# Performance work log

Measured on AMD Instinct MI355X. Metric: run time of the kernel, lower is better.

## Reference

```python
import jax, jax.numpy as jnp
import numpy as np

D_MODEL = 1024
NHEAD = 16
HEAD_DIM = D_MODEL // NHEAD
D_FF = 4096
EPS = 1e-5


def _linear(x, w, b):
    # torch Linear: y = x @ W^T + b, W is [out, in]
    return x @ w.T + b


def _layernorm(x, g, b):
    mu = jnp.mean(x, axis=-1, keepdims=True)
    var = jnp.var(x, axis=-1, keepdims=True)
    return (x - mu) * jax.lax.rsqrt(var + EPS) * g + b


def setup_inputs() -> dict:
    key = jax.random.key(0)
    ks = jax.random.split(key, 16)
    s = 0.02
    inp = {
        'x': jax.random.normal(ks[0], (2048, D_MODEL), jnp.float32),
        'q_in_w': s * jax.random.normal(ks[1], (D_MODEL, D_MODEL), jnp.float32),
        'q_in_b': jnp.zeros((D_MODEL,), jnp.float32),
        'k_in_w': s * jax.random.normal(ks[2], (D_MODEL, D_MODEL), jnp.float32),
        'k_in_b': jnp.zeros((D_MODEL,), jnp.float32),
        'v_in_w': s * jax.random.normal(ks[3], (D_MODEL, D_MODEL), jnp.float32),
        'v_in_b': jnp.zeros((D_MODEL,), jnp.float32),
        'out_w': s * jax.random.normal(ks[4], (D_MODEL, D_MODEL), jnp.float32),
        'out_b': jnp.zeros((D_MODEL,), jnp.float32),
        'ffn1_w': s * jax.random.normal(ks[5], (D_FF, D_MODEL), jnp.float32),
        'ffn1_b': jnp.zeros((D_FF,), jnp.float32),
        'ffn2_w': s * jax.random.normal(ks[6], (D_MODEL, D_FF), jnp.float32),
        'ffn2_b': jnp.zeros((D_MODEL,), jnp.float32),
        'n1_g': jnp.ones((D_MODEL,), jnp.float32),
        'n1_b': jnp.zeros((D_MODEL,), jnp.float32),
        'n2_g': jnp.ones((D_MODEL,), jnp.float32),
        'n2_b': jnp.zeros((D_MODEL,), jnp.float32),
        'q_out_w': s * jax.random.normal(ks[7], (D_MODEL, D_MODEL), jnp.float32),
        'q_out_b': jnp.zeros((D_MODEL,), jnp.float32),
        'k_out_w': s * jax.random.normal(ks[8], (D_MODEL, D_MODEL), jnp.float32),
        'k_out_b': jnp.zeros((D_MODEL,), jnp.float32),
        'v_out_w': s * jax.random.normal(ks[9], (D_MODEL, D_MODEL), jnp.float32),
        'v_out_b': jnp.zeros((D_MODEL,), jnp.float32),
        'seq_length': 2048,
    }
    return inp


def reference(x, q_in_w, q_in_b, k_in_w, k_in_b, v_in_w, v_in_b,
              out_w, out_b, ffn1_w, ffn1_b, ffn2_w, ffn2_b,
              n1_g, n1_b, n2_g, n2_b,
              q_out_w, q_out_b, k_out_w, k_out_b, v_out_w, v_out_b,
              seq_length):
    S = seq_length
    # --- is_first: batched in-projections (replaces per-token loop + cat) ---
    q_buf = _linear(x, q_in_w, q_in_b)   # [S, D]
    k_buf = _linear(x, k_in_w, k_in_b)
    v_buf = _linear(x, v_in_w, v_in_b)
    prev_layer_input = x

    # --- multi-head attention (non-causal, no mask) ---
    q = q_buf.reshape(S, NHEAD, HEAD_DIM).transpose(1, 0, 2)  # [H, S, Dh]
    k = k_buf.reshape(S, NHEAD, HEAD_DIM).transpose(1, 0, 2)
    v = v_buf.reshape(S, NHEAD, HEAD_DIM).transpose(1, 0, 2)
    scale = 1.0 / np.sqrt(HEAD_DIM).astype(np.float32)
    scores = jnp.einsum('hqd,hkd->hqk', q, k) * scale        # [H, S, S]
    attn = jax.nn.softmax(scores, axis=-1)
    ctx = jnp.einsum('hqk,hkd->hqd', attn, v)                # [H, S, Dh]
    attn_output = ctx.transpose(1, 0, 2).reshape(S, D_MODEL)  # [S, D]

    # --- post-norm residual blocks (batched over tokens) ---
    h = _linear(attn_output, out_w, out_b)
    h = _layernorm(prev_layer_input + h, n1_g, n1_b)
    ff = _linear(jax.nn.relu(_linear(h, ffn1_w, ffn1_b)), ffn2_w, ffn2_b)
    y = _layernorm(h + ff, n2_g, n2_b)                        # [S, D]

    # --- not is_last: out-projections for the next layer ---
    q_next = _linear(y, q_out_w, q_out_b)
    k_next = _linear(y, k_out_w, k_out_b)
    v_next = _linear(y, v_out_w, v_out_b)
    return (q_next, k_next, v_next, y)
```

## Files before the change

### kernel.cpp

```cpp
#include <hip/hip_runtime.h>
#include <math.h>

#define SEQ   2048
#define DM    1024
#define NH    16
#define DH    64
#define DFF   4096
#define KVSPLIT 4

typedef __bf16 bf16;
using bf16x8 = __attribute__((ext_vector_type(8))) __bf16;
using f32x4  = __attribute__((ext_vector_type(4))) float;

__device__ __forceinline__ unsigned short f2bfu(float f) {
    unsigned int u = __float_as_uint(f);
    u += 0x7FFF + ((u >> 16) & 1);
    return (unsigned short)(u >> 16);
}
__device__ __forceinline__ bf16 f2bf(float f) {
    unsigned short s = f2bfu(f);
    return __builtin_bit_cast(bf16, s);
}

__device__ __forceinline__ void gll16(const bf16* g, bf16* lds_base) {
    __builtin_amdgcn_global_load_lds(
        (const __attribute__((address_space(1))) unsigned int*)g,
        (__attribute__((address_space(3))) unsigned int*)lds_base, 16, 0, 0);
}

__global__ __launch_bounds__(256) void conv_k(const float* __restrict__ src,
                                              bf16* __restrict__ dst, int n) {
    int i = (blockIdx.x * 256 + threadIdx.x) * 4;
    if (i >= n) return;
    float4 v = *(const float4*)(src + i);
    ushort4 o;
    o.x = f2bfu(v.x); o.y = f2bfu(v.y); o.z = f2bfu(v.z); o.w = f2bfu(v.w);
    *(ushort4*)((unsigned short*)dst + i) = o;
}

struct ConvSeg  { const float* src; bf16* dst; int n; };
struct ConvSegs { ConvSeg s[6]; };

__global__ __launch_bounds__(256) void conv_multi_k(ConvSegs cs) {
    ConvSeg sg = cs.s[blockIdx.y];
    int i = (blockIdx.x * 256 + threadIdx.x) * 4;
    if (i >= sg.n) return;
    float4 v = *(const float4*)(sg.src + i);
    ushort4 o;
    o.x = f2bfu(v.x); o.y = f2bfu(v.y); o.z = f2bfu(v.z); o.w = f2bfu(v.w);
    *(ushort4*)((unsigned short*)sg.dst + i) = o;
}

struct GemmPtrs {
    const bf16* W[3];
    const float* bias[3];
    float* out32[3];
    bf16*  out16[3];
};

template<int BM, int BN>
__global__ __launch_bounds__(256) void gemm_bf16_k(
    const bf16* __restrict__ A, GemmPtrs p, int N, int K, int relu)
{
    constexpr int TM = BM / 32;
    constexpr int TN = BN / 32;
    __shared__ bf16 As[BM][32];
    __shared__ bf16 Ws[BN][32];

    const int t    = threadIdx.x;
    const int lane = t & 63;
    const int wave = t >> 6;
    const int quad = lane >> 4;
    const int l15  = lane & 15;
    const int wm   = (wave >> 1) * (BM / 2);
    const int wn   = (wave & 1) * (BN / 2);
    const int m0   = blockIdx.y * BM;
    const int n0   = blockIdx.x * BN;
    const bf16* __restrict__ W = p.W[blockIdx.z];

    f32x4 acc[TM][TN];
    #pragma unroll
    for (int i = 0; i < TM; ++i)
        #pragma unroll
        for (int j = 0; j < TN; ++j)
            acc[i][j] = f32x4{0.f, 0.f, 0.f, 0.f};

    for (int k0 = 0; k0 < K; k0 += 32) {
        #pragma unroll
        for (int s = 0; s < BM / 64; ++s) {
            int base = s * 256 + wave * 64;
            int idx  = base + lane;
            gll16(A + (long)(m0 + (idx >> 2)) * K + k0 + (idx & 3) * 8,
                  &As[0][0] + (long)base * 8);
        }
        #pragma unroll
        for (int s = 0; s < BN / 64; ++s) {
            int base = s * 256 + wave * 64;
            int idx  = base + lane;
            gll16(W + (long)(n0 + (idx >> 2)) * K + k0 + (idx & 3) * 8,
                  &Ws[0][0] + (long)base * 8);
        }
        __syncthreads();

        bf16x8 a[TM], b[TN];
        #pragma unroll
        for (int i = 0; i < TM; ++i)
            a[i] = *(const bf16x8*)&As[wm + i * 16 + l15][quad * 8];
        #pragma unroll
        for (int j = 0; j < TN; ++j)
            b[j] = *(const bf16x8*)&Ws[wn + j * 16 + l15][quad * 8];
        #pragma unroll
        for (int i = 0; i < TM; ++i)
            #pragma unroll
            for (int j = 0; j < TN; ++j)
                acc[i][j] = __builtin_amdgcn_mfma_f32_16x16x32_bf16(
                    a[i], b[j], acc[i][j], 0, 0, 0);
        __syncthreads();
    }

    float* o32 = p.out32[blockIdx.z];
    bf16*  o16 = p.out16[blockIdx.z];
    const float* bias = p.bias[blockIdx.z];
    #pragma unroll
    for (int j = 0; j < TN; ++j) {
        int n = n0 + wn + j * 16 + l15;
        float bv = bias[n];
        #pragma unroll
        for (int i = 0; i < TM; ++i) {
            #pragma unroll
            for (int r = 0; r < 4; ++r) {
                int m = m0 + wm + i * 16 + quad * 4 + r;
                float v = acc[i][j][r] + bv;
                if (relu) v = fmaxf(v, 0.f);
                if (o32) o32[(long)m * N + n] = v;
                if (o16) o16[(long)m * N + n] = f2bf(v);
            }
        }
    }
}

template<int BM, int BN, int KS>
__global__ __launch_bounds__(256) void gemm_splitk_k(
    const bf16* __restrict__ A, const bf16* __restrict__ W,
    float* __restrict__ part, int N, int K)
{
    constexpr int TM = BM / 32;
    constexpr int TN = BN / 32;
    __shared__ bf16 As[BM][32];
    __shared__ bf16 Ws[BN][32];

    const int t    = threadIdx.x;
    const int lane = t & 63;
    const int wave = t >> 6;
    const int quad = lane >> 4;
    const int l15  = lane & 15;
    const int wm   = (wave >> 1) * (BM / 2);
    const int wn   = (wave & 1) * (BN / 2);
    const int m0   = blockIdx.y * BM;
    const int n0   = blockIdx.x * BN;
    const int Kp   = K / KS;
    const int klo  = blockIdx.z * Kp;
    const long MN  = (long)gridDim.y * BM * N;

    f32x4 acc[TM][TN];
    #pragma unroll
    for (int i = 0; i < TM; ++i)
        #pragma unroll
        for (int j = 0; j < TN; ++j)
            acc[i][j] = f32x4{0.f, 0.f, 0.f, 0.f};

    for (int k0 = klo; k0 < klo + Kp; k0 += 32) {
        #pragma unroll
        for (int s = 0; s < BM / 64; ++s) {
            int base = s * 256 + wave * 64;
            int idx  = base + lane;
            gll16(A + (long)(m0 + (idx >> 2)) * K + k0 + (idx & 3) * 8,
                  &As[0][0] + (long)base * 8);
        }
        #pragma unroll
        for (int s = 0; s < BN / 64; ++s) {
            int base = s * 256 + wave * 64;
            int idx  = base + lane;
            gll16(W + (long)(n0 + (idx >> 2)) * K + k0 + (idx & 3) * 8,
                  &Ws[0][0] + (long)base * 8);
        }
        __syncthreads();

        bf16x8 a[TM], b[TN];
        #pragma unroll
        for (int i = 0; i < TM; ++i)
            a[i] = *(const bf16x8*)&As[wm + i * 16 + l15][quad * 8];
        #pragma unroll
        for (int j = 0; j < TN; ++j)
            b[j] = *(const bf16x8*)&Ws[wn + j * 16 + l15][quad * 8];
        #pragma unroll
        for (int i = 0; i < TM; ++i)
            #pragma unroll
            for (int j = 0; j < TN; ++j)
                acc[i][j] = __builtin_amdgcn_mfma_f32_16x16x32_bf16(
                    a[i], b[j], acc[i][j], 0, 0, 0);
        __syncthreads();
    }

    float* o = part + (long)blockIdx.z * MN;
    #pragma unroll
    for (int j = 0; j < TN; ++j) {
        int n = n0 + wn + j * 16 + l15;
        #pragma unroll
        for (int i = 0; i < TM; ++i)
            #pragma unroll
            for (int r = 0; r < 4; ++r) {
                int m = m0 + wm + i * 16 + quad * 4 + r;
                o[(long)m * N + n] = acc[i][j][r];
            }
    }
}

__global__ __launch_bounds__(256) void attn_mfma_k(
    const bf16* __restrict__ Q, const bf16* __restrict__ Kg,
    const bf16* __restrict__ Vg, bf16* __restrict__ Opart,
    float* __restrict__ lpart)
{
    __shared__ bf16 Kb[64][72];
    __shared__ bf16 Vt[64][72];
    __shared__ bf16 Pw[4][16][76];

    const int t    = threadIdx.x;
    const int lane = t & 63;
    const int wave = t >> 6;
    const int quad = lane >> 4;
    const int l15  = lane & 15;
    const int h    = blockIdx.y;
    const int q0   = blockIdx.x * 64;
    const int spl  = blockIdx.z;
    const int cb   = h * DH;
    const long SD  = (long)SEQ * DM;

    const int qrow = q0 + wave * 16 + l15;
    bf16x8 aQ[2];
    #pragma unroll
    for (int kh = 0; kh < 2; ++kh)
        aQ[kh] = *(const bf16x8*)(Q + (long)qrow * DM + cb + kh * 32 + quad * 8);

    bf16 oneb = f2bf(l15 == 0 ? 1.0f : 0.0f);
    bf16x8 bOnes;
    #pragma unroll
    for (int j = 0; j < 8; ++j) bOnes[j] = oneb;

    f32x4 o_acc[4], l_acc;
    #pragma unroll
    for (int dt = 0; dt < 4; ++dt) o_acc[dt] = f32x4{0.f, 0.f, 0.f, 0.f};
    l_acc = f32x4{0.f, 0.f, 0.f, 0.f};

    const float SCL = 0.18033688f;
    const int kv_lo = spl * (SEQ / KVSPLIT);
    const int kv_hi = kv_lo + SEQ / KVSPLIT;

    for (int kv0 = kv_lo; kv0 < kv_hi; kv0 += 64) {
        __syncthreads();
        #pragma unroll
        for (int s = 0; s < 2; ++s) {
            int idx = t + s * 256;
            int key = idx >> 3;
            int dg  = idx & 7;
            *(uint4*)&Kb[key][dg * 8] =
                *(const uint4*)(Kg + (long)(kv0 + key) * DM + cb + dg * 8);
            bf16x8 vv = *(const bf16x8*)(Vg + (long)(kv0 + key) * DM + cb + dg * 8);
            int swz = key ^ (dg * 8);
            #pragma unroll
            for (int j = 0; j < 8; ++j) Vt[dg * 8 + j][swz] = vv[j];
        }
        __syncthreads();

        f32x4 s4[4];
        #pragma unroll
        for (int kt = 0; kt < 4; ++kt) {
            bf16x8 b0 = *(const bf16x8*)&Kb[kt * 16 + l15][quad * 8];
            bf16x8 b1 = *(const bf16x8*)&Kb[kt * 16 + l15][32 + quad * 8];
            f32x4 s = f32x4{0.f, 0.f, 0.f, 0.f};
            s = __builtin_amdgcn_mfma_f32_16x16x32_bf16(aQ[0], b0, s, 0, 0, 0);
            s = __builtin_amdgcn_mfma_f32_16x16x32_bf16(aQ[1], b1, s, 0, 0, 0);
            s4[kt] = s;
        }

        #pragma unroll
        for (int kt = 0; kt < 4; ++kt) {
            #pragma unroll
            for (int r = 0; r < 4; ++r) {
                float pv = exp2f(s4[kt][r] * SCL);
                unsigned u = __float_as_uint(pv) + 0x8000u;
                Pw[wave][quad * 4 + r][kt * 16 + l15] =
                    __builtin_bit_cast(bf16, (unsigned short)(u >> 16));
            }
        }
        bf16x8 aP[2];
        aP[0] = *(const bf16x8*)&Pw[wave][l15][quad * 8];
        aP[1] = *(const bf16x8*)&Pw[wave][l15][32 + quad * 8];

        l_acc = __builtin_amdgcn_mfma_f32_16x16x32_bf16(aP[0], bOnes, l_acc, 0, 0, 0);
        l_acc = __builtin_amdgcn_mfma_f32_16x16x32_bf16(aP[1], bOnes, l_acc, 0, 0, 0);

        #pragma unroll
        for (int dt = 0; dt < 4; ++dt) {
            int d   = dt * 16 + l15;
            int dgr = d >> 3;
            bf16x8 v0 = *(const bf16x8*)&Vt[d][((quad) ^ dgr) * 8];
            bf16x8 v1 = *(const bf16x8*)&Vt[d][((4 + quad) ^ dgr) * 8];
            o_acc[dt] = __builtin_amdgcn_mfma_f32_16x16x32_bf16(aP[0], v0, o_acc[dt], 0, 0, 0);
            o_acc[dt] = __builtin_amdgcn_mfma_f32_16x16x32_bf16(aP[1], v1, o_acc[dt], 0, 0, 0);
        }
    }

    #pragma unroll
    for (int r = 0; r < 4; ++r) {
        int row = q0 + wave * 16 + quad * 4 + r;
        #pragma unroll
        for (int dt = 0; dt < 4; ++dt)
            Opart[(long)spl * SD + (long)row * DM + cb + dt * 16 + l15] =
                f2bf(o_acc[dt][r]);
        if (l15 == 0)
            lpart[((long)spl * NH + h) * SEQ + row] = l_acc[r];
    }
}

__global__ __launch_bounds__(256) void attn_reduce_k(
    const bf16* __restrict__ Opart, const float* __restrict__ lpart,
    bf16* __restrict__ O)
{
    const long SD = (long)SEQ * DM;
    long i = ((long)blockIdx.x * 256 + threadIdx.x) * 8;
    int row = (int)(i / DM);
    int h   = (int)((i % DM) / DH);

    float l = 0.f;
    #pragma unroll
    for (int k = 0; k < KVSPLIT; ++k)
        l += lpart[((long)k * NH + h) * SEQ + row];
    float inv = 1.f / l;

    float acc[8] = {};
    #pragma unroll
    for (int k = 0; k < KVSPLIT; ++k) {
        bf16x8 v = *(const bf16x8*)(Opart + (long)k * SD + i);
        #pragma unroll
        for (int j = 0; j < 8; ++j) acc[j] += (float)v[j];
    }
    bf16x8 o;
    #pragma unroll
    for (int j = 0; j < 8; ++j) o[j] = f2bf(acc[j] * inv);
    *(bf16x8*)(O + i) = o;
}

template<int NS>
__global__ __launch_bounds__(256) void ln_red_k(
    const float* __restrict__ part, const float* __restrict__ bias,
    const float* __restrict__ res, const float* __restrict__ g,
    const float* __restrict__ b, float* __restrict__ out32,
    bf16* __restrict__ out16)
{
    const long SD = (long)SEQ * DM;
    const int row = blockIdx.x;
    const int t   = threadIdx.x;
    const long off = (long)row * DM + (t << 2);

    float4 v = *(const float4*)(res + off);
    float4 bv0 = *(const float4*)(bias + (t << 2));
    v.x += bv0.x; v.y += bv0.y; v.z += bv0.z; v.w += bv0.w;
    #pragma unroll
    for (int z = 0; z < NS; ++z) {
        float4 pz = *(const float4*)(part + z * SD + off);
        v.x += pz.x; v.y += pz.y; v.z += pz.z; v.w += pz.w;
    }

    float s1 = v.x + v.y + v.z + v.w;
    float s2 = v.x * v.x + v.y * v.y + v.z * v.z + v.w * v.w;
    #pragma unroll
    for (int off2 = 32; off2 > 0; off2 >>= 1) {
        s1 += __shfl_xor(s1, off2);
        s2 += __shfl_xor(s2, off2);
    }
    __shared__ float red[8];
    int wid = t >> 6, lid = t & 63;
    if (lid == 0) { red[wid] = s1; red[4 + wid] = s2; }
    __syncthreads();
    s1 = red[0] + red[1] + red[2] + red[3];
    s2 = red[4] + red[5] + red[6] + red[7];

    float mu   = s1 * (1.f / DM);
    float var  = s2 * (1.f / DM) - mu * mu;
    float rstd = rsqrtf(var + 1e-5f);

    float4 gv = *(const float4*)(g + (t << 2));
    float4 bv = *(const float4*)(b + (t << 2));
    float4 ov;
    ov.x = (v.x - mu) * rstd * gv.x + bv.x;
    ov.y = (v.y - mu) * rstd * gv.y + bv.y;
    ov.z = (v.z - mu) * rstd * gv.z + bv.z;
    ov.w = (v.w - mu) * rstd * gv.w + bv.w;
    if (out32) *(float4*)(out32 + off) = ov;
    if (out16) {
        ushort4 o;
        o.x = f2bfu(ov.x); o.y = f2bfu(ov.y); o.z = f2bfu(ov.z); o.w = f2bfu(ov.w);
        *(ushort4*)((unsigned short*)out16 + off) = o;
    }
}

extern "C" void kernel_launch(void* const* d_in, const int* in_sizes, int n_in,
                              void* d_out, int out_size, void* d_ws, size_t ws_size,
                              hipStream_t stream)
{
    const float* x       = (const float*)d_in[0];
    const float* q_in_w  = (const float*)d_in[1];
    const float* q_in_b  = (const float*)d_in[2];
    const float* k_in_w  = (const float*)d_in[3];
    const float* k_in_b  = (const float*)d_in[4];
    const float* v_in_w  = (const float*)d_in[5];
    const float* v_in_b  = (const float*)d_in[6];
    const float* out_w   = (const float*)d_in[7];
    const float* out_b   = (const float*)d_in[8];
    const float* ffn1_w  = (const float*)d_in[9];
    const float* ffn1_b  = (const float*)d_in[10];
    const float* ffn2_w  = (const float*)d_in[11];
    const float* ffn2_b  = (const float*)d_in[12];
    const float* n1_g    = (const float*)d_in[13];
    const float* n1_b    = (const float*)d_in[14];
    const float* n2_g    = (const float*)d_in[15];
    const float* n2_b    = (const float*)d_in[16];
    const float* q_out_w = (const float*)d_in[17];
    const float* q_out_b = (const float*)d_in[18];
    const float* k_out_w = (const float*)d_in[19];
    const float* k_out_b = (const float*)d_in[20];
    const float* v_out_w = (const float*)d_in[21];
    const float* v_out_b = (const float*)d_in[22];

    float* out = (float*)d_out;
    const long SD = (long)SEQ * DM;
    const long MB = 1024 * 1024;

    char* w = (char*)d_ws;
    bf16*  xbf   = (bf16*)(w);
    float* lpart = (float*)(w);
    bf16*  qb    = (bf16*)(w + 4  * MB);
    bf16*  kb    = (bf16*)(w + 8  * MB);
    bf16*  vb    = (bf16*)(w + 12 * MB);
    bf16*  atnb  = (bf16*)(w + 16 * MB);
    float* h32   = (float*)(w);
    bf16*  h16   = (bf16*)(w + 8  * MB);
    float* P2    = (float*)(w + 8  * MB);
    bf16*  Opart = (bf16*)(w + 20 * MB);
    float* P1    = (float*)(w + 20 * MB);
    bf16*  f1    = (bf16*)(w + 24 * MB);
    bf16*  wqi   = (bf16*)(w + 32 * MB);
    bf16*  wki   = (bf16*)(w + 34 * MB);
    bf16*  wvi   = (bf16*)(w + 36 * MB);
    bf16*  wo    = (bf16*)(w + 38 * MB);
    bf16*  wf1   = (bf16*)(w + 40 * MB);
    bf16*  wf2   = (bf16*)(w + 40 * MB);
    bf16*  wqo   = (bf16*)(w + 24 * MB);
    bf16*  wko   = (bf16*)(w + 26 * MB);
    bf16*  wvo   = (bf16*)(w + 28 * MB);
    bf16*  ybf   = (bf16*)(w + 30 * MB);
    float* y32   = out + 3 * SD;

    dim3 blk(256);
    const int DD = DM * DM;

    {
        ConvSegs cs;
        cs.s[0] = {x,      xbf, (int)SD};
        cs.s[1] = {q_in_w, wqi, DD};
        cs.s[2] = {k_in_w, wki, DD};
        cs.s[3] = {v_in_w, wvi, DD};
        cs.s[4] = {out_w,  wo,  DD};
        cs.s[5] = {ffn1_w, wf1, DM * DFF};
        conv_multi_k<<<dim3(DM * DFF / 1024, 6), blk, 0, stream>>>(cs);
    }

    {
        GemmPtrs p{};
        p.W[0] = wqi; p.W[1] = wki; p.W[2] = wvi;
        p.bias[0] = q_in_b; p.bias[1] = k_in_b; p.bias[2] = v_in_b;
        p.out16[0] = qb; p.out16[1] = kb; p.out16[2] = vb;
        gemm_bf16_k<128, 64><<<dim3(DM / 64, SEQ / 128, 3), blk, 0, stream>>>(
            xbf, p, DM, DM, 0);
    }

    attn_mfma_k<<<dim3(SEQ / 64, NH, KVSPLIT), blk, 0, stream>>>(
        qb, kb, vb, Opart, lpart);
    attn_reduce_k<<<dim3((int)(SD / 2048)), blk, 0, stream>>>(Opart, lpart, atnb);

    gemm_splitk_k<64, 128, 2><<<dim3(DM / 128, SEQ / 64, 2), blk, 0, stream>>>(
        atnb, wo, P1, DM, DM);

    ln_red_k<2><<<SEQ, blk, 0, stream>>>(P1, out_b, x, n1_g, n1_b, h32, h16);

    {
        GemmPtrs p{};
        p.W[0] = wf1; p.bias[0] = ffn1_b; p.out16[0] = f1;
        gemm_bf16_k<128, 64><<<dim3(DFF / 64, SEQ / 128, 1), blk, 0, stream>>>(
            h16, p, DFF, DM, 1);
    }

    conv_k<<<dim3(DM * DFF / 1024), blk, 0, stream>>>(ffn2_w, wf2, DM * DFF);

    gemm_splitk_k<64, 128, 2><<<dim3(DM / 128, SEQ / 64, 2), blk, 0, stream>>>(
        f1, wf2, P2, DM, DFF);

    {
        ConvSegs cs;
        cs.s[0] = {q_out_w, wqo, DD};
        cs.s[1] = {k_out_w, wko, DD};
        cs.s[2] = {v_out_w, wvo, DD};
        cs.s[3] = cs.s[0]; cs.s[4] = cs.s[0]; cs.s[5] = cs.s[0];
        conv_multi_k<<<dim3(DD / 1024, 3), blk, 0, stream>>>(cs);
    }

    ln_red_k<2><<<SEQ, blk, 0, stream>>>(P2, ffn2_b, h32, n2_g, n2_b, y32, ybf);

    {
        GemmPtrs p{};
        p.W[0] = wqo; p.W[1] = wko; p.W[2] = wvo;
        p.bias[0] = q_out_b; p.bias[1] = k_out_b; p.bias[2] = v_out_b;
        p.out32[0] = out; p.out32[1] = out + SD; p.out32[2] = out + 2 * SD;
        gemm_bf16_k<128, 64><<<dim3(DM / 64, SEQ / 128, 3), blk, 0, stream>>>(
            ybf, p, DM, DM, 0);
    }
}
```

Measured before the change: 356.9 us.

## Compute transposed scores in registers to drop K and P shared-memory staging

The attention kernel now computes S^T by putting K as the MFMA A operand, loaded straight from global memory, and Q as the B operand. The score fragments are then already in the register layout the P·V MFMA needs, so the P round-trip through shared memory and the K shared-memory tile go away. The V shared-memory layout is permuted on write to match the new key ordering. The row sum comes from register adds plus cross-lane shuffles instead of an extra MFMA against a ones vector. In exchange, K is re-read from global or cache by every wave and the P operand is converted per element in registers.

```diff
diff --git a/kernel.cpp b/kernel.cpp
--- a/kernel.cpp
+++ b/kernel.cpp
@@ -221,9 +221,7 @@
     const bf16* __restrict__ Vg, bf16* __restrict__ Opart,
     float* __restrict__ lpart)
 {
-    __shared__ bf16 Kb[64][72];
     __shared__ bf16 Vt[64][72];
-    __shared__ bf16 Pw[4][16][76];
 
     const int t    = threadIdx.x;
     const int lane = t & 63;
@@ -237,20 +235,15 @@
     const long SD  = (long)SEQ * DM;
 
     const int qrow = q0 + wave * 16 + l15;
-    bf16x8 aQ[2];
+    bf16x8 bQ[2];
     #pragma unroll
     for (int kh = 0; kh < 2; ++kh)
-        aQ[kh] = *(const bf16x8*)(Q + (long)qrow * DM + cb + kh * 32 + quad * 8);
-
-    bf16 oneb = f2bf(l15 == 0 ? 1.0f : 0.0f);
-    bf16x8 bOnes;
-    #pragma unroll
-    for (int j = 0; j < 8; ++j) bOnes[j] = oneb;
-
-    f32x4 o_acc[4], l_acc;
+        bQ[kh] = *(const bf16x8*)(Q + (long)qrow * DM + cb + kh * 32 + quad * 8);
+
+    f32x4 o_acc[4];
     #pragma unroll
     for (int dt = 0; dt < 4; ++dt) o_acc[dt] = f32x4{0.f, 0.f, 0.f, 0.f};
-    l_acc = f32x4{0.f, 0.f, 0.f, 0.f};
+    float lsum = 0.f;
 
     const float SCL = 0.18033688f;
     const int kv_lo = spl * (SEQ / KVSPLIT);
@@ -263,48 +256,42 @@
             int idx = t + s * 256;
             int key = idx >> 3;
             int dg  = idx & 7;
-            *(uint4*)&Kb[key][dg * 8] =
-                *(const uint4*)(Kg + (long)(kv0 + key) * DM + cb + dg * 8);
             bf16x8 vv = *(const bf16x8*)(Vg + (long)(kv0 + key) * DM + cb + dg * 8);
-            int swz = key ^ (dg * 8);
+            int vk  = (key & 0x20) | ((key & 0x0f) << 1) | ((key & 0x10) >> 4);
+            int swz = vk ^ (dg * 8);
             #pragma unroll
             for (int j = 0; j < 8; ++j) Vt[dg * 8 + j][swz] = vv[j];
         }
         __syncthreads();
 
-        f32x4 s4[4];
+        float p[16];
         #pragma unroll
         for (int kt = 0; kt < 4; ++kt) {
-            bf16x8 b0 = *(const bf16x8*)&Kb[kt * 16 + l15][quad * 8];
-            bf16x8 b1 = *(const bf16x8*)&Kb[kt * 16 + l15][32 + quad * 8];
-            f32x4 s = f32x4{0.f, 0.f, 0.f, 0.f};
-            s = __builtin_amdgcn_mfma_f32_16x16x32_bf16(aQ[0], b0, s, 0, 0, 0);
-            s = __builtin_amdgcn_mfma_f32_16x16x32_bf16(aQ[1], b1, s, 0, 0, 0);
-            s4[kt] = s;
-        }
-
-        #pragma unroll
-        for (int kt = 0; kt < 4; ++kt) {
-            #pragma unroll
-            for (int r = 0; r < 4; ++r) {
-                float pv = exp2f(s4[kt][r] * SCL);
-                unsigned u = __float_as_uint(pv) + 0x8000u;
-                Pw[wave][quad * 4 + r][kt * 16 + l15] =
-                    __builtin_bit_cast(bf16, (unsigned short)(u >> 16));
+            const bf16* kp = Kg + (long)(kv0 + kt * 16 + l15) * DM + cb + quad * 8;
+            bf16x8 a0 = *(const bf16x8*)kp;
+            bf16x8 a1 = *(const bf16x8*)(kp + 32);
+            f32x4 sv = f32x4{0.f, 0.f, 0.f, 0.f};
+            sv = __builtin_amdgcn_mfma_f32_16x16x32_bf16(a0, bQ[0], sv, 0, 0, 0);
+            sv = __builtin_amdgcn_mfma_f32_16x16x32_bf16(a1, bQ[1], sv, 0, 0, 0);
+            #pragma unroll
+            for (int r = 0; r < 4; ++r) p[kt * 4 + r] = exp2f(sv[r] * SCL);
+        }
+
+        bf16x8 aP[2];
+        #pragma unroll
+        for (int c = 0; c < 2; ++c)
+            #pragma unroll
+            for (int j = 0; j < 8; ++j) {
+                float pv = p[(2 * c + (j & 1)) * 4 + (j >> 1)];
+                lsum += pv;
+                aP[c][j] = f2bf(pv);
             }
-        }
-        bf16x8 aP[2];
-        aP[0] = *(const bf16x8*)&Pw[wave][l15][quad * 8];
-        aP[1] = *(const bf16x8*)&Pw[wave][l15][32 + quad * 8];
-
-        l_acc = __builtin_amdgcn_mfma_f32_16x16x32_bf16(aP[0], bOnes, l_acc, 0, 0, 0);
-        l_acc = __builtin_amdgcn_mfma_f32_16x16x32_bf16(aP[1], bOnes, l_acc, 0, 0, 0);
 
         #pragma unroll
         for (int dt = 0; dt < 4; ++dt) {
             int d   = dt * 16 + l15;
             int dgr = d >> 3;
-            bf16x8 v0 = *(const bf16x8*)&Vt[d][((quad) ^ dgr) * 8];
+            bf16x8 v0 = *(const bf16x8*)&Vt[d][(quad ^ dgr) * 8];
             bf16x8 v1 = *(const bf16x8*)&Vt[d][((4 + quad) ^ dgr) * 8];
             o_acc[dt] = __builtin_amdgcn_mfma_f32_16x16x32_bf16(aP[0], v0, o_acc[dt], 0, 0, 0);
             o_acc[dt] = __builtin_amdgcn_mfma_f32_16x16x32_bf16(aP[1], v1, o_acc[dt], 0, 0, 0);
@@ -318,9 +305,11 @@
         for (int dt = 0; dt < 4; ++dt)
             Opart[(long)spl * SD + (long)row * DM + cb + dt * 16 + l15] =
                 f2bf(o_acc[dt][r]);
-        if (l15 == 0)
-            lpart[((long)spl * NH + h) * SEQ + row] = l_acc[r];
-    }
+    }
+    lsum += __shfl_xor(lsum, 16);
+    lsum += __shfl_xor(lsum, 32);
+    if (quad == 0)
+        lpart[((long)spl * NH + h) * SEQ + qrow] = lsum;
 }
 
 __global__ __launch_bounds__(256) void attn_reduce_k(
```

Result: slower. 386.5 us (+8.3%).
